# Kernel tuning notes

Hardware: AMD Instinct MI355X
Metric: run time of the kernel (lower is better)

## Reference

```python
import jax, jax.numpy as jnp
import numpy as np

N_NODES = 50000
N_EDGES = 1600000
IN_FEATS = 256
OUT_FEATS = 128
NEG_SLOPE = 0.2


def setup_inputs() -> dict:
    key = jax.random.key(0)
    k1, k2, k3, k4, k5, k6 = jax.random.split(key, 6)
    gain = np.sqrt(2.0)  # calculate_gain('relu')
    w_std = gain * np.sqrt(2.0 / (IN_FEATS + OUT_FEATS))  # xavier normal
    a_std = gain * np.sqrt(2.0 / (1 + OUT_FEATS))
    return {
        "feat": jax.random.normal(k1, (N_NODES, IN_FEATS), dtype=jnp.float32),
        "W": jax.random.normal(k2, (OUT_FEATS, IN_FEATS), dtype=jnp.float32) * w_std,
        "attn_l": jax.random.normal(k3, (1, OUT_FEATS), dtype=jnp.float32) * a_std,
        "attn_r": jax.random.normal(k4, (1, OUT_FEATS), dtype=jnp.float32) * a_std,
        "src": jax.random.randint(k5, (N_EDGES,), 0, N_NODES, dtype=jnp.int32),
        "dst": jax.random.randint(k6, (N_EDGES,), 0, N_NODES, dtype=jnp.int32),
    }


def reference(feat, W, attn_l, attn_r, src, dst):
    # h = fc(feat): [N, D]
    h = jnp.einsum("ni,di->nd", feat, W)
    # per-node attention logits
    el = jnp.sum(h * attn_l, axis=-1)  # [N]
    er = jnp.sum(h * attn_r, axis=-1)  # [N]
    # apply_edge: e_uv = el[u] + er[v], then leaky relu
    e = jax.nn.leaky_relu(el[src] + er[dst], NEG_SLOPE)  # [E]
    # edge softmax over incoming edges of each destination node
    m = jax.ops.segment_max(e, dst, num_segments=N_NODES)  # [N]
    m = jnp.where(jnp.isneginf(m), 0.0, m)  # nodes with no in-edges
    ex = jnp.exp(e - m[dst])  # [E]
    denom = jax.ops.segment_sum(ex, dst, num_segments=N_NODES)  # [N]
    alpha = ex / jnp.maximum(denom[dst], 1e-9)  # [E]
    # gspmv: rst[v] = sum_{(u->v)} alpha_uv * h[u]
    rst = jax.ops.segment_sum(h[src] * alpha[:, None], dst, num_segments=N_NODES)
    return rst
```

## Files before the change

### kernel.cpp

```cpp
#include <hip/hip_runtime.h>
#include <hip/hip_bf16.h>


#define IN_FEATS 256
#define OUT_FEATS 128
#define NBINS 256
#define CAPB_LOG 14
#define CAPB (1 << CAPB_LOG)
#define SCAT_BLOCKS 1024

typedef __bf16 bf16x8 __attribute__((ext_vector_type(8)));
typedef float f32x4 __attribute__((ext_vector_type(4)));

__global__ void cast_w(const float* __restrict__ W, __bf16* __restrict__ Wb, int n) {
    int i = blockIdx.x * blockDim.x + threadIdx.x;
    if (i < n) Wb[i] = (__bf16)W[i];
}

__global__ void init_cursor(int* __restrict__ cur) {
    int i = blockIdx.x * blockDim.x + threadIdx.x;
    if (i < NBINS) cur[i] = i << CAPB_LOG;
}

__global__ __launch_bounds__(256) void gemm_mfma(const float* __restrict__ feat,
                                                 const __bf16* __restrict__ Wb,
                                                 const float* __restrict__ attn_l,
                                                 const float* __restrict__ attn_r,
                                                 __bf16* __restrict__ hb,
                                                 float* __restrict__ el,
                                                 float* __restrict__ er, int n) {
    const int wid = threadIdx.x >> 6;
    const int lane = threadIdx.x & 63;
    const int s = lane & 15;
    const int q = lane >> 4;
    const int m0 = blockIdx.x * 64 + wid * 16;
    if (m0 >= n) return;

    const int mrow = min(m0 + s, n - 1);
    const float* arow = feat + (size_t)mrow * IN_FEATS + q * 8;

    f32x4 acc[8];
#pragma unroll
    for (int nt = 0; nt < 8; nt++) acc[nt] = (f32x4){0.f, 0.f, 0.f, 0.f};

#pragma unroll
    for (int ks = 0; ks < 8; ks++) {
        const int k0 = ks * 32;
        float4 f0 = *(const float4*)(arow + k0);
        float4 f1 = *(const float4*)(arow + k0 + 4);
        bf16x8 a;
        a[0] = (__bf16)f0.x; a[1] = (__bf16)f0.y; a[2] = (__bf16)f0.z; a[3] = (__bf16)f0.w;
        a[4] = (__bf16)f1.x; a[5] = (__bf16)f1.y; a[6] = (__bf16)f1.z; a[7] = (__bf16)f1.w;
#pragma unroll
        for (int nt = 0; nt < 8; nt++) {
            bf16x8 b = *(const bf16x8*)(Wb + (size_t)(nt * 16 + s) * IN_FEATS + k0 + q * 8);
            acc[nt] = __builtin_amdgcn_mfma_f32_16x16x32_bf16(a, b, acc[nt], 0, 0, 0);
        }
    }

    float al[8], ar[8];
#pragma unroll
    for (int nt = 0; nt < 8; nt++) {
        al[nt] = attn_l[nt * 16 + s];
        ar[nt] = attn_r[nt * 16 + s];
    }

#pragma unroll
    for (int r = 0; r < 4; r++) {
        const int row = m0 + q * 4 + r;
        const bool ok = row < n;
        float pl = 0.f, pr = 0.f;
#pragma unroll
        for (int nt = 0; nt < 8; nt++) {
            float v = acc[nt][r];
            if (ok) hb[(size_t)row * OUT_FEATS + nt * 16 + s] = (__bf16)v;
            pl += v * al[nt];
            pr += v * ar[nt];
        }
#pragma unroll
        for (int m = 1; m < 16; m <<= 1) {
            pl += __shfl_xor(pl, m);
            pr += __shfl_xor(pr, m);
        }
        if (ok && s == 0) {
            el[row] = pl;
            er[row] = pr;
        }
    }
}

__global__ __launch_bounds__(256) void scatter_kernel(const int* __restrict__ src,
                                                      const int* __restrict__ dst,
                                                      int* __restrict__ bin_cur,
                                                      unsigned* __restrict__ arena,
                                                      int E) {
    __shared__ int h[NBINS];
    __shared__ int base[NBINS];
    const int t = threadIdx.x;
    h[t] = 0;
    __syncthreads();
    const int chunk = (E + gridDim.x - 1) / gridDim.x;
    const int beg = blockIdx.x * chunk;
    const int end = min(beg + chunk, E);
    for (int i = beg + t; i < end; i += 256)
        atomicAdd(&h[dst[i] >> 8], 1);
    __syncthreads();
    if (h[t] > 0)
        base[t] = atomicAdd(&bin_cur[t], h[t]);
    h[t] = 0;
    __syncthreads();
    for (int i = beg + t; i < end; i += 256) {
        int d = dst[i];
        int bin = d >> 8;
        int pos = base[bin] + atomicAdd(&h[bin], 1);
        pos = min(pos, ((bin + 1) << CAPB_LOG) - 1);
        arena[pos] = ((unsigned)d << 16) | (unsigned)src[i];
    }
}

__global__ __launch_bounds__(256) void build_csr(const unsigned* __restrict__ arena,
                                                 const int* __restrict__ bin_cur,
                                                 unsigned* __restrict__ edges,
                                                 int* __restrict__ row_beg,
                                                 int* __restrict__ row_end,
                                                 int N) {
    __shared__ int cnt[256];
    __shared__ int off[256];
    const int b = blockIdx.x;
    const int t = threadIdx.x;
    const int beg = b << CAPB_LOG;
    const int end = min(bin_cur[b], (b + 1) << CAPB_LOG);

    cnt[t] = 0;
    __syncthreads();
    for (int i = beg + t; i < end; i += 256)
        atomicAdd(&cnt[(arena[i] >> 16) & 255], 1);
    __syncthreads();
    const int mycnt = cnt[t];
    off[t] = mycnt;
    __syncthreads();
    for (int o = 1; o < 256; o <<= 1) {
        int v = (t >= o) ? off[t - o] : 0;
        __syncthreads();
        off[t] += v;
        __syncthreads();
    }
    const int excl = off[t] - mycnt;
    __syncthreads();
    off[t] = excl;
    __syncthreads();

    const int v = (b << 8) + t;
    if (v < N) {
        row_beg[v] = beg + excl;
        row_end[v] = beg + excl + mycnt;
    }

    cnt[t] = 0;
    __syncthreads();
    for (int i = beg + t; i < end; i += 256) {
        unsigned e = arena[i];
        int d8 = (e >> 16) & 255;
        int r = atomicAdd(&cnt[d8], 1);
        edges[beg + off[d8] + r] = e;
    }
}

__global__ __launch_bounds__(256) void gat_kernel(const __bf16* __restrict__ hb,
                                                  const float* __restrict__ el,
                                                  const float* __restrict__ er,
                                                  const unsigned* __restrict__ edges,
                                                  const int* __restrict__ row_beg,
                                                  const int* __restrict__ row_end,
                                                  float* __restrict__ out, int n) {
    const int v = blockIdx.x * 4 + (threadIdx.x >> 6);
    if (v >= n) return;
    const int lane = threadIdx.x & 63;
    const int beg = row_beg[v];
    const int end = row_end[v];
    const float erv = er[v];
    const unsigned* hbu = (const unsigned*)hb;

    float acc0 = 0.f, acc1 = 0.f, wsum = 0.f;
    for (int c0 = beg; c0 < end; c0 += 64) {
        const int nn = min(64, end - c0);
        int u_my = (c0 + lane < end) ? (int)(edges[c0 + lane] & 0xFFFFu) : 0;
        float e = el[u_my] + erv;
        e = (e > 0.f) ? e : 0.2f * e;
        float w_my = __expf(e);

        int k = 0;
        for (; k + 4 <= nn; k += 4) {
#pragma unroll
            for (int tt = 0; tt < 4; tt++) {
                int u = __shfl(u_my, k + tt);
                float w = __shfl(w_my, k + tt);
                wsum += w;
                unsigned pair = hbu[(size_t)u * (OUT_FEATS / 2) + lane];
                acc0 += w * __uint_as_float(pair << 16);
                acc1 += w * __uint_as_float(pair & 0xffff0000u);
            }
        }
        for (; k < nn; k++) {
            int u = __shfl(u_my, k);
            float w = __shfl(w_my, k);
            wsum += w;
            unsigned pair = hbu[(size_t)u * (OUT_FEATS / 2) + lane];
            acc0 += w * __uint_as_float(pair << 16);
            acc1 += w * __uint_as_float(pair & 0xffff0000u);
        }
    }
    const float dnm = fmaxf(wsum, 1e-9f);
    float2 o = make_float2(acc0 / dnm, acc1 / dnm);
    *(float2*)(out + (size_t)v * OUT_FEATS + lane * 2) = o;
}

extern "C" void kernel_launch(void* const* d_in, const int* in_sizes, int n_in,
                              void* d_out, int out_size, void* d_ws, size_t ws_size,
                              hipStream_t stream) {
    const float* feat   = (const float*)d_in[0];
    const float* W      = (const float*)d_in[1];
    const float* attn_l = (const float*)d_in[2];
    const float* attn_r = (const float*)d_in[3];
    const int*   src    = (const int*)d_in[4];
    const int*   dst    = (const int*)d_in[5];
    const int N = in_sizes[0] / IN_FEATS;
    const int E = in_sizes[4];
    float* out = (float*)d_out;

    char* p = (char*)d_ws;
    auto alloc = [&](size_t bytes) -> char* {
        char* r = p;
        p += (bytes + 255) & ~(size_t)255;
        return r;
    };
    __bf16* hb    = (__bf16*)alloc((size_t)N * OUT_FEATS * sizeof(__bf16));
    __bf16* Wb    = (__bf16*)alloc((size_t)OUT_FEATS * IN_FEATS * sizeof(__bf16));
    float* el     = (float*)alloc((size_t)N * sizeof(float));
    float* er     = (float*)alloc((size_t)N * sizeof(float));
    int*   bin_cur = (int*)alloc((size_t)NBINS * sizeof(int));
    int*   row_beg = (int*)alloc((size_t)N * sizeof(int));
    int*   row_end = (int*)alloc((size_t)N * sizeof(int));
    unsigned* arena = (unsigned*)alloc((size_t)NBINS * CAPB * sizeof(unsigned));
    unsigned* edges = (unsigned*)alloc((size_t)NBINS * CAPB * sizeof(unsigned));

    const int nbuckets = (N + 255) / 256;

    cast_w<<<dim3((OUT_FEATS * IN_FEATS + 255) / 256), dim3(256), 0, stream>>>(
        W, Wb, OUT_FEATS * IN_FEATS);
    init_cursor<<<dim3(1), dim3(256), 0, stream>>>(bin_cur);

    gemm_mfma<<<dim3((N + 63) / 64), dim3(256), 0, stream>>>(feat, Wb, attn_l, attn_r,
                                                             hb, el, er, N);

    scatter_kernel<<<dim3(SCAT_BLOCKS), dim3(256), 0, stream>>>(src, dst, bin_cur,
                                                                arena, E);
    build_csr<<<dim3(nbuckets), dim3(256), 0, stream>>>(arena, bin_cur, edges,
                                                        row_beg, row_end, N);

    gat_kernel<<<dim3((N + 3) / 4), dim3(256), 0, stream>>>(hb, el, er, edges,
                                                            row_beg, row_end, out, N);
}
```

Before: 247.7 us.

## Precompute edge weights in CSR build and split bins into slices

Each bucket's CSR build is split into 8 slice blocks of 32 destinations, which raises parallelism. The build now computes the leaky-ReLU and exp edge weight and packs its upper 16 bits (a bf16-truncated value) with the source index into each edge word. The aggregation kernel then skips the el gather and the exp and reads weight and index from one word. It also merges the cast and cursor-init kernels into one and halves the scatter block count. The trade-offs are that each slice block rescans the whole bin (8x arena reads), weights lose precision, and slices hold a fixed 2048 entries, so overflow is clamped.

```diff
diff --git a/kernel.cpp b/kernel.cpp
--- a/kernel.cpp
+++ b/kernel.cpp
@@ -7,18 +7,17 @@
 #define NBINS 256
 #define CAPB_LOG 14
 #define CAPB (1 << CAPB_LOG)
-#define SCAT_BLOCKS 1024
+#define SCAT_BLOCKS 512
+#define SLICE_DSTS 32
+#define SCAP 2048
 
 typedef __bf16 bf16x8 __attribute__((ext_vector_type(8)));
 typedef float f32x4 __attribute__((ext_vector_type(4)));
 
-__global__ void cast_w(const float* __restrict__ W, __bf16* __restrict__ Wb, int n) {
-    int i = blockIdx.x * blockDim.x + threadIdx.x;
-    if (i < n) Wb[i] = (__bf16)W[i];
-}
-
-__global__ void init_cursor(int* __restrict__ cur) {
-    int i = blockIdx.x * blockDim.x + threadIdx.x;
+__global__ void prep(const float* __restrict__ W, __bf16* __restrict__ Wb, int nw,
+                     int* __restrict__ cur) {
+    int i = blockIdx.x * 256 + threadIdx.x;
+    if (i < nw) Wb[i] = (__bf16)W[i];
     if (i < NBINS) cur[i] = i << CAPB_LOG;
 }
 
@@ -120,55 +119,72 @@
 
 __global__ __launch_bounds__(256) void build_csr(const unsigned* __restrict__ arena,
                                                  const int* __restrict__ bin_cur,
+                                                 const float* __restrict__ el,
+                                                 const float* __restrict__ er,
                                                  unsigned* __restrict__ edges,
                                                  int* __restrict__ row_beg,
                                                  int* __restrict__ row_end,
-                                                 int N) {
-    __shared__ int cnt[256];
-    __shared__ int off[256];
-    const int b = blockIdx.x;
+                                                 int N, int edges_cap) {
+    __shared__ int cnt[SLICE_DSTS];
+    __shared__ int off[SLICE_DSTS];
+    const int blk = blockIdx.x;
+    const int b = blk >> 3;
+    const int j = blk & 7;
     const int t = threadIdx.x;
-    const int beg = b << CAPB_LOG;
-    const int end = min(bin_cur[b], (b + 1) << CAPB_LOG);
-
-    cnt[t] = 0;
-    __syncthreads();
-    for (int i = beg + t; i < end; i += 256)
-        atomicAdd(&cnt[(arena[i] >> 16) & 255], 1);
-    __syncthreads();
-    const int mycnt = cnt[t];
-    off[t] = mycnt;
-    __syncthreads();
-    for (int o = 1; o < 256; o <<= 1) {
-        int v = (t >= o) ? off[t - o] : 0;
+    const int abeg = b << CAPB_LOG;
+    const int aend = min(bin_cur[b], abeg + CAPB);
+
+    if (t < SLICE_DSTS) cnt[t] = 0;
+    __syncthreads();
+    for (int i = abeg + t; i < aend; i += 256) {
+        int d8 = (arena[i] >> 16) & 255;
+        if ((d8 >> 5) == j) atomicAdd(&cnt[d8 & 31], 1);
+    }
+    __syncthreads();
+    if (t < SLICE_DSTS) off[t] = cnt[t];
+    __syncthreads();
+    for (int o = 1; o < SLICE_DSTS; o <<= 1) {
+        int v = (t >= o && t < SLICE_DSTS) ? off[t - o] : 0;
         __syncthreads();
-        off[t] += v;
+        if (t < SLICE_DSTS) off[t] += v;
         __syncthreads();
     }
-    const int excl = off[t] - mycnt;
-    __syncthreads();
-    off[t] = excl;
-    __syncthreads();
-
-    const int v = (b << 8) + t;
-    if (v < N) {
-        row_beg[v] = beg + excl;
-        row_end[v] = beg + excl + mycnt;
-    }
-
-    cnt[t] = 0;
-    __syncthreads();
-    for (int i = beg + t; i < end; i += 256) {
+    int mycnt = 0, excl = 0;
+    if (t < SLICE_DSTS) {
+        mycnt = cnt[t];
+        excl = off[t] - mycnt;
+    }
+    __syncthreads();
+    if (t < SLICE_DSTS) off[t] = excl;
+    __syncthreads();
+
+    const int sbase = blk * SCAP;
+    if (t < SLICE_DSTS) {
+        int v = (b << 8) + j * SLICE_DSTS + t;
+        if (v < N) {
+            row_beg[v] = sbase + excl;
+            row_end[v] = sbase + excl + mycnt;
+        }
+        cnt[t] = 0;
+    }
+    __syncthreads();
+    for (int i = abeg + t; i < aend; i += 256) {
         unsigned e = arena[i];
         int d8 = (e >> 16) & 255;
-        int r = atomicAdd(&cnt[d8], 1);
-        edges[beg + off[d8] + r] = e;
+        if ((d8 >> 5) != j) continue;
+        int u = (int)(e & 0xFFFFu);
+        int d = (b << 8) + d8;
+        float x = el[u] + er[d];
+        x = (x > 0.f) ? x : 0.2f * x;
+        float w = __expf(x);
+        int r = atomicAdd(&cnt[d8 & 31], 1);
+        int pos = sbase + off[d8 & 31] + r;
+        pos = min(pos, edges_cap - 1);
+        edges[pos] = (__float_as_uint(w) & 0xFFFF0000u) | (unsigned)u;
     }
 }
 
 __global__ __launch_bounds__(256) void gat_kernel(const __bf16* __restrict__ hb,
-                                                  const float* __restrict__ el,
-                                                  const float* __restrict__ er,
                                                   const unsigned* __restrict__ edges,
                                                   const int* __restrict__ row_beg,
                                                   const int* __restrict__ row_end,
@@ -178,23 +194,20 @@
     const int lane = threadIdx.x & 63;
     const int beg = row_beg[v];
     const int end = row_end[v];
-    const float erv = er[v];
     const unsigned* hbu = (const unsigned*)hb;
 
     float acc0 = 0.f, acc1 = 0.f, wsum = 0.f;
     for (int c0 = beg; c0 < end; c0 += 64) {
         const int nn = min(64, end - c0);
-        int u_my = (c0 + lane < end) ? (int)(edges[c0 + lane] & 0xFFFFu) : 0;
-        float e = el[u_my] + erv;
-        e = (e > 0.f) ? e : 0.2f * e;
-        float w_my = __expf(e);
+        int my = (c0 + lane < end) ? (int)edges[c0 + lane] : 0;
 
         int k = 0;
         for (; k + 4 <= nn; k += 4) {
 #pragma unroll
             for (int tt = 0; tt < 4; tt++) {
-                int u = __shfl(u_my, k + tt);
-                float w = __shfl(w_my, k + tt);
+                unsigned e = (unsigned)__shfl(my, k + tt);
+                int u = (int)(e & 0xFFFFu);
+                float w = __uint_as_float(e & 0xFFFF0000u);
                 wsum += w;
                 unsigned pair = hbu[(size_t)u * (OUT_FEATS / 2) + lane];
                 acc0 += w * __uint_as_float(pair << 16);
@@ -202,8 +215,9 @@
             }
         }
         for (; k < nn; k++) {
-            int u = __shfl(u_my, k);
-            float w = __shfl(w_my, k);
+            unsigned e = (unsigned)__shfl(my, k);
+            int u = (int)(e & 0xFFFFu);
+            float w = __uint_as_float(e & 0xFFFF0000u);
             wsum += w;
             unsigned pair = hbu[(size_t)u * (OUT_FEATS / 2) + lane];
             acc0 += w * __uint_as_float(pair << 16);
@@ -234,6 +248,10 @@
         p += (bytes + 255) & ~(size_t)255;
         return r;
     };
+    const int nbuckets = (N + 255) / 256;
+    const int nslices = nbuckets * 8;
+    const int edges_cap = nslices * SCAP;
+
     __bf16* hb    = (__bf16*)alloc((size_t)N * OUT_FEATS * sizeof(__bf16));
     __bf16* Wb    = (__bf16*)alloc((size_t)OUT_FEATS * IN_FEATS * sizeof(__bf16));
     float* el     = (float*)alloc((size_t)N * sizeof(float));
@@ -242,22 +260,19 @@
     int*   row_beg = (int*)alloc((size_t)N * sizeof(int));
     int*   row_end = (int*)alloc((size_t)N * sizeof(int));
     unsigned* arena = (unsigned*)alloc((size_t)NBINS * CAPB * sizeof(unsigned));
-    unsigned* edges = (unsigned*)alloc((size_t)NBINS * CAPB * sizeof(unsigned));
-
-    const int nbuckets = (N + 255) / 256;
-
-    cast_w<<<dim3((OUT_FEATS * IN_FEATS + 255) / 256), dim3(256), 0, stream>>>(
-        W, Wb, OUT_FEATS * IN_FEATS);
-    init_cursor<<<dim3(1), dim3(256), 0, stream>>>(bin_cur);
+    unsigned* edges = (unsigned*)alloc((size_t)edges_cap * sizeof(unsigned));
+
+    prep<<<dim3((OUT_FEATS * IN_FEATS + 255) / 256), dim3(256), 0, stream>>>(
+        W, Wb, OUT_FEATS * IN_FEATS, bin_cur);
 
     gemm_mfma<<<dim3((N + 63) / 64), dim3(256), 0, stream>>>(feat, Wb, attn_l, attn_r,
                                                              hb, el, er, N);
 
     scatter_kernel<<<dim3(SCAT_BLOCKS), dim3(256), 0, stream>>>(src, dst, bin_cur,
                                                                 arena, E);
-    build_csr<<<dim3(nbuckets), dim3(256), 0, stream>>>(arena, bin_cur, edges,
-                                                        row_beg, row_end, N);
-
-    gat_kernel<<<dim3((N + 3) / 4), dim3(256), 0, stream>>>(hb, el, er, edges,
-                                                            row_beg, row_end, out, N);
-}
+    build_csr<<<dim3(nslices), dim3(256), 0, stream>>>(arena, bin_cur, el, er, edges,
+                                                       row_beg, row_end, N, edges_cap);
+
+    gat_kernel<<<dim3((N + 3) / 4), dim3(256), 0, stream>>>(hb, edges, row_beg,
+                                                            row_end, out, N);
+}
```

New measurement: 252.5 us. Within noise of the previous version (+1.9%).
